# Kernel tuning notes

Measured on AMD Instinct MI355X. Metric: run time of the kernel, lower is better.

The kernel has to match this reference:

```python
import jax, jax.numpy as jnp
import numpy as np

ALPHA = 0.2  # LeakyReLU negative slope


def gat_layer(x, W, a, alpha=ALPHA):
    """Multi-head dense GAT layer.
    x: (B, N, F); W: (H, F, O); a: (H, 2*O, 1).
    Returns (B, N, H*O) — ELU(head outputs) concatenated over heads.
    """
    H, F, O = W.shape
    Wh = jnp.einsum('bnf,hfo->bhno', x, W)          # (B,H,N,O)
    a_src = a[:, :O, 0]                              # (H,O)
    a_dst = a[:, O:, 0]                              # (H,O)
    s_src = jnp.einsum('bhno,ho->bhn', Wh, a_src)    # (B,H,N)
    s_dst = jnp.einsum('bhno,ho->bhn', Wh, a_dst)    # (B,H,N)
    e = s_src[..., :, None] + s_dst[..., None, :]    # (B,H,N,N)
    e = jax.nn.leaky_relu(e, negative_slope=alpha)
    att = jax.nn.softmax(e, axis=-1)                 # softmax over neighbors j
    out = jnp.einsum('bhnm,bhmo->bhno', att, Wh)     # (B,H,N,O)
    out = jax.nn.elu(out)
    B, _, N, _ = out.shape
    return jnp.transpose(out, (0, 2, 1, 3)).reshape(B, N, H * O)


def setup_inputs() -> dict:
    key = jax.random.key(0)
    ks = jax.random.split(key, 5)
    B, N = 32, 1024
    x = jax.random.normal(ks[0], (B, N, 4), dtype=jnp.float32)
    # layer1: nfeat=4, nhid=2, nheads=3
    W1 = jax.random.normal(ks[1], (3, 4, 2), dtype=jnp.float32) * 0.5
    a1 = jax.random.normal(ks[2], (3, 4, 1), dtype=jnp.float32) * 0.5
    # layer2: nfeat=6, nhid=4, nheads=1
    W2 = jax.random.normal(ks[3], (1, 6, 4), dtype=jnp.float32) * 0.5
    a2 = jax.random.normal(ks[4], (1, 8, 1), dtype=jnp.float32) * 0.5
    return {"x": x, "W1": W1, "a1": a1, "W2": W2, "a2": a2}


def reference(x, W1, a1, W2, a2):
    h = gat_layer(x, W1, a1)   # (B, N, 6)
    y = gat_layer(h, W2, a2)   # (B, N, 4)
    return y
```

## Files before the change

### kernel.cpp

```cpp
#include <hip/hip_runtime.h>


#define GAT_ALPHA 0.2f
#define LOG2E 1.44269504088896f

__device__ __forceinline__ float ex2(float v) { return __builtin_amdgcn_exp2f(v); }

template <int F, int O, int H, int NT>
__global__ __launch_bounds__(NT) void gat_bucket_kernel(
    const float* __restrict__ x,
    const float* __restrict__ Wt,
    const float* __restrict__ at,
    float* __restrict__ out)
{
    constexpr int N = 1024, EPT = N / NT;
    constexpr int NB = 512;
    constexpr int A1 = O + 1;
    constexpr int NW = NT / 64;
    constexpr int NJOBS = 2 * A1 + 1;
    constexpr int BPL = NB / 64;

    const int bid = blockIdx.x;
    const int h   = bid % H;
    const int b   = bid / H;
    const int tid = threadIdx.x;
    const int wv  = tid >> 6, ln = tid & 63;

    float Wl[F][O], asrc[O], adst[O];
#pragma unroll
    for (int f = 0; f < F; ++f)
#pragma unroll
        for (int o = 0; o < O; ++o) Wl[f][o] = Wt[(h * F + f) * O + o];
#pragma unroll
    for (int o = 0; o < O; ++o) {
        asrc[o] = at[h * 2 * O + o];
        adst[o] = at[h * 2 * O + O + o];
    }

    __shared__ float sSrc[N];
    __shared__ int   sCS[NB + 1];
    __shared__ float sKey[N];
    __shared__ float sWhS[O][N];
    __shared__ float sPre[A1][NB + 1];
    __shared__ float sSuf[A1][NB + 1];
    __shared__ float sMM[2 * NW];

    for (int i = tid; i < NB + 1; i += NT) sCS[i] = 0;
    for (int i = tid; i < A1 * (NB + 1); i += NT) {
        (&sPre[0][0])[i] = 0.0f;
        (&sSuf[0][0])[i] = 0.0f;
    }

    float key[EPT], wh[EPT][O];
    float kmin = 3.4e38f, kmax = -3.4e38f;
    const float* xb = x + (size_t)b * N * F;
#pragma unroll
    for (int k = 0; k < EPT; ++k) {
        const int m = k * NT + tid;
        float xv[F];
        if constexpr (F == 4) {
            const float4 v = ((const float4*)xb)[m];
            xv[0] = v.x; xv[1] = v.y; xv[2] = v.z; xv[3] = v.w;
        } else {
            const float2* x2 = (const float2*)xb;
            const float2 va = x2[3 * m], vb = x2[3 * m + 1], vc = x2[3 * m + 2];
            xv[0] = va.x; xv[1] = va.y; xv[2] = vb.x;
            xv[3] = vb.y; xv[4] = vc.x; xv[5] = vc.y;
        }
        float d = 0.0f, sn = 0.0f;
#pragma unroll
        for (int o = 0; o < O; ++o) {
            float acc = 0.0f;
#pragma unroll
            for (int f = 0; f < F; ++f) acc += xv[f] * Wl[f][o];
            wh[k][o] = acc;
            d += acc * adst[o];
            sn += acc * asrc[o];
        }
        key[k] = d;
        sSrc[m] = sn;
        kmin = fminf(kmin, d);
        kmax = fmaxf(kmax, d);
    }
#pragma unroll
    for (int s = 1; s < 64; s <<= 1) {
        kmin = fminf(kmin, __shfl_xor(kmin, s, 64));
        kmax = fmaxf(kmax, __shfl_xor(kmax, s, 64));
    }
    if (ln == 0) { sMM[wv] = kmin; sMM[NW + wv] = kmax; }
    __syncthreads();

    kmin = sMM[0]; kmax = sMM[NW];
#pragma unroll
    for (int w = 1; w < NW; ++w) {
        kmin = fminf(kmin, sMM[w]);
        kmax = fmaxf(kmax, sMM[NW + w]);
    }
    const float invw = (float)NB / fmaxf(kmax - kmin, 1e-30f);

    int bk[EPT], rk[EPT];
#pragma unroll
    for (int k = 0; k < EPT; ++k) {
        int q = (int)((key[k] - kmin) * invw);
        q = q < 0 ? 0 : (q > NB - 1 ? NB - 1 : q);
        bk[k] = q;
        rk[k] = atomicAdd(&sCS[q], 1);
        const float e1 = ex2(LOG2E * key[k]);
        const float e2 = ex2(GAT_ALPHA * LOG2E * key[k]);
        atomicAdd(&sSuf[0][q], e1);
        atomicAdd(&sPre[0][q], e2);
#pragma unroll
        for (int o = 0; o < O; ++o) {
            atomicAdd(&sSuf[1 + o][q], e1 * wh[k][o]);
            atomicAdd(&sPre[1 + o][q], e2 * wh[k][o]);
        }
    }
    __syncthreads();

    if (wv < NJOBS) {
        if (wv == 0) {
            int c[BPL];
#pragma unroll
            for (int i = 0; i < BPL; ++i) c[i] = sCS[ln * BPL + i];
            int s = 0;
#pragma unroll
            for (int i = 0; i < BPL; ++i) s += c[i];
            int run = s;
#pragma unroll
            for (int d = 1; d < 64; d <<= 1) {
                const int u = __shfl_up(run, d, 64);
                if (ln >= d) run += u;
            }
            int acc = run - s;
#pragma unroll
            for (int i = 0; i < BPL; ++i) {
                const int t = acc; acc += c[i];
                sCS[ln * BPL + i] = t;
            }
            if (ln == 0) sCS[NB] = N;
        } else if (wv <= A1) {
            float* arr = &sPre[wv - 1][0];
            float v[BPL];
#pragma unroll
            for (int i = 0; i < BPL; ++i) v[i] = arr[ln * BPL + i];
            float s = 0.0f;
#pragma unroll
            for (int i = 0; i < BPL; ++i) s += v[i];
            float run = s;
#pragma unroll
            for (int d = 1; d < 64; d <<= 1) {
                const float u = __shfl_up(run, d, 64);
                if (ln >= d) run += u;
            }
            float acc = run - s;
#pragma unroll
            for (int i = 0; i < BPL; ++i) {
                const float t = acc; acc += v[i];
                arr[ln * BPL + i] = t;
            }
        } else {
            float* arr = &sSuf[wv - A1 - 1][0];
            float v[BPL];
#pragma unroll
            for (int i = 0; i < BPL; ++i) v[i] = arr[ln * BPL + i];
            float s = 0.0f;
#pragma unroll
            for (int i = 0; i < BPL; ++i) s += v[i];
            float run = s;
#pragma unroll
            for (int d = 1; d < 64; d <<= 1) {
                const float u = __shfl_down(run, d, 64);
                if (ln < 64 - d) run += u;
            }
            float acc = run - s;
#pragma unroll
            for (int i = BPL - 1; i >= 0; --i) {
                acc += v[i];
                arr[ln * BPL + i] = acc;
            }
        }
    }
    __syncthreads();

#pragma unroll
    for (int k = 0; k < EPT; ++k) {
        const int pos = sCS[bk[k]] + rk[k];
        sKey[pos] = key[k];
#pragma unroll
        for (int o = 0; o < O; ++o) sWhS[o][pos] = wh[k][o];
    }
    __syncthreads();

    for (int rr = tid; rr < N; rr += NT) {
        const float sn = sSrc[rr];
        const float rho = ex2(0.8f * LOG2E * sn);
        int bq = (int)((-sn - kmin) * invw);
        bq = bq < 0 ? 0 : (bq > NB - 1 ? NB - 1 : bq);
        const int i0 = sCS[bq], i1 = sCS[bq + 1];
        float den = rho * sSuf[0][bq + 1] + sPre[0][bq];
        float num[O];
#pragma unroll
        for (int o = 0; o < O; ++o)
            num[o] = rho * sSuf[1 + o][bq + 1] + sPre[1 + o][bq];
        for (int i = i0; i < i1; ++i) {
            const float kk = sKey[i];
            const float w = fmaxf(rho * ex2(LOG2E * kk), ex2(GAT_ALPHA * LOG2E * kk));
            den += w;
#pragma unroll
            for (int o = 0; o < O; ++o) num[o] += w * sWhS[o][i];
        }
#pragma unroll
        for (int o = 0; o < O; ++o) {
            float v = num[o] / den;
            v = (v > 0.0f) ? v : (__expf(v) - 1.0f);
            out[((size_t)b * N + rr) * (H * O) + h * O + o] = v;
        }
    }
}

extern "C" void kernel_launch(void* const* d_in, const int* in_sizes, int n_in,
                              void* d_out, int out_size, void* d_ws, size_t ws_size,
                              hipStream_t stream) {
    const float* x  = (const float*)d_in[0];
    const float* W1 = (const float*)d_in[1];
    const float* a1 = (const float*)d_in[2];
    const float* W2 = (const float*)d_in[3];
    const float* a2 = (const float*)d_in[4];

    float* h1 = (float*)d_ws;
    float* y  = (float*)d_out;

    constexpr int B = 32;
    gat_bucket_kernel<4, 2, 3, 1024><<<B * 3, 1024, 0, stream>>>(x, W1, a1, h1);
    gat_bucket_kernel<6, 4, 1, 1024><<<B * 1, 1024, 0, stream>>>(h1, W2, a2, y);
}
```

Baseline: 91.51 us.

## Fuse both GAT layers into one per-batch kernel with aliased shared memory

Merges the two layer launches into a single kernel with one block per batch element. That block computes all three layer-1 heads, keeps the layer-1 output in registers, and then runs layer 2, so the global-memory round trip of the hidden activations and one launch go away. In layer 1 the bucket stage stores only sorted node indices and recomputes Wh and the key from x inside the within-bucket loop, which saves shared memory so three heads fit and layer 2 can reuse the same region. The cost is parallelism: only 32 blocks run instead of 96 for layer 1, which leaves most CUs idle, and the recompute adds gathered global reads in the inner loop.

Result: slower. 114.2 us (+24.8%).

```diff
diff --git a/kernel.cpp b/kernel.cpp
--- a/kernel.cpp
+++ b/kernel.cpp
@@ -6,215 +6,323 @@
 
 __device__ __forceinline__ float ex2(float v) { return __builtin_amdgcn_exp2f(v); }
 
-template <int F, int O, int H, int NT>
-__global__ __launch_bounds__(NT) void gat_bucket_kernel(
+constexpr int N = 1024, NT = 1024, NW = NT / 64, NB = 512, BPL = NB / 64;
+constexpr int WCS = NB + 1;
+
+constexpr int OFF_PRE1 = WCS;
+constexpr int OFF_SUF1 = OFF_PRE1 + 3 * WCS;
+constexpr int OFF_IDX1 = OFF_SUF1 + 3 * WCS;
+constexpr int L1_HEAD  = OFF_IDX1 + N;
+constexpr int L1_ZERO  = OFF_IDX1;
+constexpr int SMEM_WORDS = 3 * L1_HEAD;
+
+constexpr int OFF2_KEY = WCS;
+constexpr int OFF2_WHS = OFF2_KEY + N;
+constexpr int OFF2_PRE = OFF2_WHS + 4 * N;
+constexpr int OFF2_SUF = OFF2_PRE + 5 * WCS;
+constexpr int L2_TOTAL = OFF2_SUF + 5 * WCS;
+static_assert(L2_TOTAL <= SMEM_WORDS, "L2 must alias inside L1 region");
+
+__device__ __forceinline__ void wave_scan_int(int* a, int ln) {
+    int c[BPL];
+#pragma unroll
+    for (int i = 0; i < BPL; ++i) c[i] = a[ln * BPL + i];
+    int s = 0;
+#pragma unroll
+    for (int i = 0; i < BPL; ++i) s += c[i];
+    int run = s;
+#pragma unroll
+    for (int d = 1; d < 64; d <<= 1) {
+        const int u = __shfl_up(run, d, 64);
+        if (ln >= d) run += u;
+    }
+    int acc = run - s;
+#pragma unroll
+    for (int i = 0; i < BPL; ++i) { const int t = acc; acc += c[i]; a[ln * BPL + i] = t; }
+    if (ln == 63) a[NB] = run;
+}
+__device__ __forceinline__ void wave_scan_pre(float* a, int ln) {
+    float c[BPL];
+#pragma unroll
+    for (int i = 0; i < BPL; ++i) c[i] = a[ln * BPL + i];
+    float s = 0.0f;
+#pragma unroll
+    for (int i = 0; i < BPL; ++i) s += c[i];
+    float run = s;
+#pragma unroll
+    for (int d = 1; d < 64; d <<= 1) {
+        const float u = __shfl_up(run, d, 64);
+        if (ln >= d) run += u;
+    }
+    float acc = run - s;
+#pragma unroll
+    for (int i = 0; i < BPL; ++i) { const float t = acc; acc += c[i]; a[ln * BPL + i] = t; }
+}
+__device__ __forceinline__ void wave_scan_suf(float* a, int ln) {
+    float c[BPL];
+#pragma unroll
+    for (int i = 0; i < BPL; ++i) c[i] = a[ln * BPL + i];
+    float s = 0.0f;
+#pragma unroll
+    for (int i = 0; i < BPL; ++i) s += c[i];
+    float run = s;
+#pragma unroll
+    for (int d = 1; d < 64; d <<= 1) {
+        const float u = __shfl_down(run, d, 64);
+        if (ln < 64 - d) run += u;
+    }
+    float acc = run - s;
+#pragma unroll
+    for (int i = BPL - 1; i >= 0; --i) { acc += c[i]; a[ln * BPL + i] = acc; }
+}
+
+__global__ __launch_bounds__(NT) void gat_fused(
     const float* __restrict__ x,
-    const float* __restrict__ Wt,
-    const float* __restrict__ at,
+    const float* __restrict__ W1,
+    const float* __restrict__ a1,
+    const float* __restrict__ W2,
+    const float* __restrict__ a2,
     float* __restrict__ out)
 {
-    constexpr int N = 1024, EPT = N / NT;
-    constexpr int NB = 512;
-    constexpr int A1 = O + 1;
-    constexpr int NW = NT / 64;
-    constexpr int NJOBS = 2 * A1 + 1;
-    constexpr int BPL = NB / 64;
-
-    const int bid = blockIdx.x;
-    const int h   = bid % H;
-    const int b   = bid / H;
-    const int tid = threadIdx.x;
-    const int wv  = tid >> 6, ln = tid & 63;
-
-    float Wl[F][O], asrc[O], adst[O];
-#pragma unroll
-    for (int f = 0; f < F; ++f)
-#pragma unroll
-        for (int o = 0; o < O; ++o) Wl[f][o] = Wt[(h * F + f) * O + o];
-#pragma unroll
-    for (int o = 0; o < O; ++o) {
-        asrc[o] = at[h * 2 * O + o];
-        adst[o] = at[h * 2 * O + O + o];
-    }
-
-    __shared__ float sSrc[N];
-    __shared__ int   sCS[NB + 1];
-    __shared__ float sKey[N];
-    __shared__ float sWhS[O][N];
-    __shared__ float sPre[A1][NB + 1];
-    __shared__ float sSuf[A1][NB + 1];
-    __shared__ float sMM[2 * NW];
-
-    for (int i = tid; i < NB + 1; i += NT) sCS[i] = 0;
-    for (int i = tid; i < A1 * (NB + 1); i += NT) {
-        (&sPre[0][0])[i] = 0.0f;
-        (&sSuf[0][0])[i] = 0.0f;
-    }
-
-    float key[EPT], wh[EPT][O];
-    float kmin = 3.4e38f, kmax = -3.4e38f;
-    const float* xb = x + (size_t)b * N * F;
-#pragma unroll
-    for (int k = 0; k < EPT; ++k) {
-        const int m = k * NT + tid;
-        float xv[F];
-        if constexpr (F == 4) {
-            const float4 v = ((const float4*)xb)[m];
-            xv[0] = v.x; xv[1] = v.y; xv[2] = v.z; xv[3] = v.w;
-        } else {
-            const float2* x2 = (const float2*)xb;
-            const float2 va = x2[3 * m], vb = x2[3 * m + 1], vc = x2[3 * m + 2];
-            xv[0] = va.x; xv[1] = va.y; xv[2] = vb.x;
-            xv[3] = vb.y; xv[4] = vc.x; xv[5] = vc.y;
-        }
-        float d = 0.0f, sn = 0.0f;
-#pragma unroll
-        for (int o = 0; o < O; ++o) {
-            float acc = 0.0f;
-#pragma unroll
-            for (int f = 0; f < F; ++f) acc += xv[f] * Wl[f][o];
-            wh[k][o] = acc;
-            d += acc * adst[o];
-            sn += acc * asrc[o];
-        }
-        key[k] = d;
-        sSrc[m] = sn;
-        kmin = fminf(kmin, d);
-        kmax = fmaxf(kmax, d);
-    }
-#pragma unroll
-    for (int s = 1; s < 64; s <<= 1) {
-        kmin = fminf(kmin, __shfl_xor(kmin, s, 64));
-        kmax = fmaxf(kmax, __shfl_xor(kmax, s, 64));
-    }
-    if (ln == 0) { sMM[wv] = kmin; sMM[NW + wv] = kmax; }
-    __syncthreads();
-
-    kmin = sMM[0]; kmax = sMM[NW];
-#pragma unroll
-    for (int w = 1; w < NW; ++w) {
-        kmin = fminf(kmin, sMM[w]);
-        kmax = fmaxf(kmax, sMM[NW + w]);
-    }
-    const float invw = (float)NB / fmaxf(kmax - kmin, 1e-30f);
-
-    int bk[EPT], rk[EPT];
-#pragma unroll
-    for (int k = 0; k < EPT; ++k) {
-        int q = (int)((key[k] - kmin) * invw);
+    __shared__ __align__(16) float smem[SMEM_WORDS];
+    __shared__ float sMM[4][2 * NW];
+
+    const int b   = blockIdx.x;
+    const int tid = threadIdx.x, wv = tid >> 6, ln = tid & 63;
+    const int m   = tid;
+
+    float Wl1[3][4][2], as1[3][2], ad1[3][2];
+#pragma unroll
+    for (int hh = 0; hh < 3; ++hh) {
+#pragma unroll
+        for (int f = 0; f < 4; ++f)
+#pragma unroll
+            for (int o = 0; o < 2; ++o) Wl1[hh][f][o] = W1[(hh * 4 + f) * 2 + o];
+#pragma unroll
+        for (int o = 0; o < 2; ++o) {
+            as1[hh][o] = a1[hh * 4 + o];
+            ad1[hh][o] = a1[hh * 4 + 2 + o];
+        }
+    }
+
+    const float4* xb4 = (const float4*)(x + (size_t)b * N * 4);
+
+#pragma unroll
+    for (int hh = 0; hh < 3; ++hh) {
+        float* bp = smem + hh * L1_HEAD;
+        for (int i = tid; i < L1_ZERO; i += NT) bp[i] = 0.0f;
+    }
+
+    const float4 xr = xb4[m];
+    float key1[3], sn1[3], wh1[3][2];
+#pragma unroll
+    for (int hh = 0; hh < 3; ++hh) {
+        const float w0 = xr.x * Wl1[hh][0][0] + xr.y * Wl1[hh][1][0] +
+                         xr.z * Wl1[hh][2][0] + xr.w * Wl1[hh][3][0];
+        const float w1 = xr.x * Wl1[hh][0][1] + xr.y * Wl1[hh][1][1] +
+                         xr.z * Wl1[hh][2][1] + xr.w * Wl1[hh][3][1];
+        wh1[hh][0] = w0; wh1[hh][1] = w1;
+        key1[hh] = w0 * ad1[hh][0] + w1 * ad1[hh][1];
+        sn1[hh]  = w0 * as1[hh][0] + w1 * as1[hh][1];
+        float mn = key1[hh], mx = key1[hh];
+#pragma unroll
+        for (int d = 1; d < 64; d <<= 1) {
+            mn = fminf(mn, __shfl_xor(mn, d, 64));
+            mx = fmaxf(mx, __shfl_xor(mx, d, 64));
+        }
+        if (ln == 0) { sMM[hh][wv] = mn; sMM[hh][NW + wv] = mx; }
+    }
+    __syncthreads();
+
+    float kmin1[3], invw1[3];
+#pragma unroll
+    for (int hh = 0; hh < 3; ++hh) {
+        float mn = sMM[hh][0], mx = sMM[hh][NW];
+#pragma unroll
+        for (int w = 1; w < NW; ++w) {
+            mn = fminf(mn, sMM[hh][w]);
+            mx = fmaxf(mx, sMM[hh][NW + w]);
+        }
+        kmin1[hh] = mn;
+        invw1[hh] = (float)NB / fmaxf(mx - mn, 1e-30f);
+    }
+
+    int bk1[3], rk1[3];
+#pragma unroll
+    for (int hh = 0; hh < 3; ++hh) {
+        float* bp = smem + hh * L1_HEAD;
+        int q = (int)((key1[hh] - kmin1[hh]) * invw1[hh]);
         q = q < 0 ? 0 : (q > NB - 1 ? NB - 1 : q);
-        bk[k] = q;
-        rk[k] = atomicAdd(&sCS[q], 1);
-        const float e1 = ex2(LOG2E * key[k]);
-        const float e2 = ex2(GAT_ALPHA * LOG2E * key[k]);
-        atomicAdd(&sSuf[0][q], e1);
-        atomicAdd(&sPre[0][q], e2);
-#pragma unroll
-        for (int o = 0; o < O; ++o) {
-            atomicAdd(&sSuf[1 + o][q], e1 * wh[k][o]);
-            atomicAdd(&sPre[1 + o][q], e2 * wh[k][o]);
-        }
-    }
-    __syncthreads();
-
-    if (wv < NJOBS) {
-        if (wv == 0) {
-            int c[BPL];
-#pragma unroll
-            for (int i = 0; i < BPL; ++i) c[i] = sCS[ln * BPL + i];
-            int s = 0;
-#pragma unroll
-            for (int i = 0; i < BPL; ++i) s += c[i];
-            int run = s;
-#pragma unroll
-            for (int d = 1; d < 64; d <<= 1) {
-                const int u = __shfl_up(run, d, 64);
-                if (ln >= d) run += u;
-            }
-            int acc = run - s;
-#pragma unroll
-            for (int i = 0; i < BPL; ++i) {
-                const int t = acc; acc += c[i];
-                sCS[ln * BPL + i] = t;
-            }
-            if (ln == 0) sCS[NB] = N;
-        } else if (wv <= A1) {
-            float* arr = &sPre[wv - 1][0];
-            float v[BPL];
-#pragma unroll
-            for (int i = 0; i < BPL; ++i) v[i] = arr[ln * BPL + i];
-            float s = 0.0f;
-#pragma unroll
-            for (int i = 0; i < BPL; ++i) s += v[i];
-            float run = s;
-#pragma unroll
-            for (int d = 1; d < 64; d <<= 1) {
-                const float u = __shfl_up(run, d, 64);
-                if (ln >= d) run += u;
-            }
-            float acc = run - s;
-#pragma unroll
-            for (int i = 0; i < BPL; ++i) {
-                const float t = acc; acc += v[i];
-                arr[ln * BPL + i] = t;
-            }
-        } else {
-            float* arr = &sSuf[wv - A1 - 1][0];
-            float v[BPL];
-#pragma unroll
-            for (int i = 0; i < BPL; ++i) v[i] = arr[ln * BPL + i];
-            float s = 0.0f;
-#pragma unroll
-            for (int i = 0; i < BPL; ++i) s += v[i];
-            float run = s;
-#pragma unroll
-            for (int d = 1; d < 64; d <<= 1) {
-                const float u = __shfl_down(run, d, 64);
-                if (ln < 64 - d) run += u;
-            }
-            float acc = run - s;
-#pragma unroll
-            for (int i = BPL - 1; i >= 0; --i) {
-                acc += v[i];
-                arr[ln * BPL + i] = acc;
-            }
-        }
-    }
-    __syncthreads();
-
-#pragma unroll
-    for (int k = 0; k < EPT; ++k) {
-        const int pos = sCS[bk[k]] + rk[k];
-        sKey[pos] = key[k];
-#pragma unroll
-        for (int o = 0; o < O; ++o) sWhS[o][pos] = wh[k][o];
-    }
-    __syncthreads();
-
-    for (int rr = tid; rr < N; rr += NT) {
-        const float sn = sSrc[rr];
+        bk1[hh] = q;
+        rk1[hh] = atomicAdd((int*)bp + q, 1);
+        const float e1 = ex2(LOG2E * key1[hh]);
+        const float e2 = ex2(GAT_ALPHA * LOG2E * key1[hh]);
+        atomicAdd(bp + OFF_SUF1 + q, e1);
+        atomicAdd(bp + OFF_PRE1 + q, e2);
+#pragma unroll
+        for (int o = 0; o < 2; ++o) {
+            atomicAdd(bp + OFF_SUF1 + (1 + o) * WCS + q, e1 * wh1[hh][o]);
+            atomicAdd(bp + OFF_PRE1 + (1 + o) * WCS + q, e2 * wh1[hh][o]);
+        }
+    }
+    __syncthreads();
+
+    for (int job = wv; job < 21; job += NW) {
+        const int hh = job / 7, role = job % 7;
+        float* bp = smem + hh * L1_HEAD;
+        if (role == 0)      wave_scan_int((int*)bp, ln);
+        else if (role <= 3) wave_scan_pre(bp + OFF_PRE1 + (role - 1) * WCS, ln);
+        else                wave_scan_suf(bp + OFF_SUF1 + (role - 4) * WCS, ln);
+    }
+    __syncthreads();
+
+#pragma unroll
+    for (int hh = 0; hh < 3; ++hh) {
+        float* bp = smem + hh * L1_HEAD;
+        const int pos = ((int*)bp)[bk1[hh]] + rk1[hh];
+        ((int*)bp)[OFF_IDX1 + pos] = m;
+    }
+    __syncthreads();
+
+    float hv[6];
+#pragma unroll
+    for (int hh = 0; hh < 3; ++hh) {
+        float* bp = smem + hh * L1_HEAD;
+        const int* cs = (const int*)bp;
+        const float sn = sn1[hh];
         const float rho = ex2(0.8f * LOG2E * sn);
-        int bq = (int)((-sn - kmin) * invw);
+        int bq = (int)((-sn - kmin1[hh]) * invw1[hh]);
         bq = bq < 0 ? 0 : (bq > NB - 1 ? NB - 1 : bq);
-        const int i0 = sCS[bq], i1 = sCS[bq + 1];
-        float den = rho * sSuf[0][bq + 1] + sPre[0][bq];
-        float num[O];
-#pragma unroll
-        for (int o = 0; o < O; ++o)
-            num[o] = rho * sSuf[1 + o][bq + 1] + sPre[1 + o][bq];
+        const int i0 = cs[bq], i1 = cs[bq + 1];
+        float den = rho * bp[OFF_SUF1 + bq + 1] + bp[OFF_PRE1 + bq];
+        float n0  = rho * bp[OFF_SUF1 + WCS + bq + 1] + bp[OFF_PRE1 + WCS + bq];
+        float n1  = rho * bp[OFF_SUF1 + 2 * WCS + bq + 1] + bp[OFF_PRE1 + 2 * WCS + bq];
         for (int i = i0; i < i1; ++i) {
-            const float kk = sKey[i];
+            const int mi = ((const int*)bp)[OFF_IDX1 + i];
+            const float4 xi = xb4[mi];
+            const float w0 = xi.x * Wl1[hh][0][0] + xi.y * Wl1[hh][1][0] +
+                             xi.z * Wl1[hh][2][0] + xi.w * Wl1[hh][3][0];
+            const float w1 = xi.x * Wl1[hh][0][1] + xi.y * Wl1[hh][1][1] +
+                             xi.z * Wl1[hh][2][1] + xi.w * Wl1[hh][3][1];
+            const float kk = w0 * ad1[hh][0] + w1 * ad1[hh][1];
             const float w = fmaxf(rho * ex2(LOG2E * kk), ex2(GAT_ALPHA * LOG2E * kk));
             den += w;
-#pragma unroll
-            for (int o = 0; o < O; ++o) num[o] += w * sWhS[o][i];
-        }
-#pragma unroll
-        for (int o = 0; o < O; ++o) {
+            n0 += w * w0;
+            n1 += w * w1;
+        }
+        float v0 = n0 / den, v1 = n1 / den;
+        hv[hh * 2]     = (v0 > 0.0f) ? v0 : (__expf(v0) - 1.0f);
+        hv[hh * 2 + 1] = (v1 > 0.0f) ? v1 : (__expf(v1) - 1.0f);
+    }
+    __syncthreads();
+
+    float Wl2[6][4], as2[4], ad2[4];
+#pragma unroll
+    for (int f = 0; f < 6; ++f)
+#pragma unroll
+        for (int o = 0; o < 4; ++o) Wl2[f][o] = W2[f * 4 + o];
+#pragma unroll
+    for (int o = 0; o < 4; ++o) { as2[o] = a2[o]; ad2[o] = a2[4 + o]; }
+
+    for (int i = tid; i < WCS; i += NT) ((int*)smem)[i] = 0;
+    for (int i = tid; i < 10 * WCS; i += NT) smem[OFF2_PRE + i] = 0.0f;
+
+    float key2, sn2, wh2[4];
+    {
+        float kd = 0.0f, sn = 0.0f;
+#pragma unroll
+        for (int o = 0; o < 4; ++o) {
+            float acc = 0.0f;
+#pragma unroll
+            for (int f = 0; f < 6; ++f) acc += hv[f] * Wl2[f][o];
+            wh2[o] = acc;
+            kd += acc * ad2[o];
+            sn += acc * as2[o];
+        }
+        key2 = kd; sn2 = sn;
+        float mn = kd, mx = kd;
+#pragma unroll
+        for (int d = 1; d < 64; d <<= 1) {
+            mn = fminf(mn, __shfl_xor(mn, d, 64));
+            mx = fmaxf(mx, __shfl_xor(mx, d, 64));
+        }
+        if (ln == 0) { sMM[3][wv] = mn; sMM[3][NW + wv] = mx; }
+    }
+    __syncthreads();
+
+    float kmin2, invw2;
+    {
+        float mn = sMM[3][0], mx = sMM[3][NW];
+#pragma unroll
+        for (int w = 1; w < NW; ++w) {
+            mn = fminf(mn, sMM[3][w]);
+            mx = fmaxf(mx, sMM[3][NW + w]);
+        }
+        kmin2 = mn;
+        invw2 = (float)NB / fmaxf(mx - mn, 1e-30f);
+    }
+
+    int bk2, rk2;
+    {
+        int q = (int)((key2 - kmin2) * invw2);
+        q = q < 0 ? 0 : (q > NB - 1 ? NB - 1 : q);
+        bk2 = q;
+        rk2 = atomicAdd((int*)smem + q, 1);
+        const float e1 = ex2(LOG2E * key2);
+        const float e2 = ex2(GAT_ALPHA * LOG2E * key2);
+        atomicAdd(smem + OFF2_SUF + q, e1);
+        atomicAdd(smem + OFF2_PRE + q, e2);
+#pragma unroll
+        for (int o = 0; o < 4; ++o) {
+            atomicAdd(smem + OFF2_SUF + (1 + o) * WCS + q, e1 * wh2[o]);
+            atomicAdd(smem + OFF2_PRE + (1 + o) * WCS + q, e2 * wh2[o]);
+        }
+    }
+    __syncthreads();
+
+    if (wv < 11) {
+        if (wv == 0)      wave_scan_int((int*)smem, ln);
+        else if (wv <= 5) wave_scan_pre(smem + OFF2_PRE + (wv - 1) * WCS, ln);
+        else              wave_scan_suf(smem + OFF2_SUF + (wv - 6) * WCS, ln);
+    }
+    __syncthreads();
+
+    {
+        const int pos = ((int*)smem)[bk2] + rk2;
+        smem[OFF2_KEY + pos] = key2;
+#pragma unroll
+        for (int o = 0; o < 4; ++o) smem[OFF2_WHS + o * N + pos] = wh2[o];
+    }
+    __syncthreads();
+
+    {
+        const int* cs = (const int*)smem;
+        const float rho = ex2(0.8f * LOG2E * sn2);
+        int bq = (int)((-sn2 - kmin2) * invw2);
+        bq = bq < 0 ? 0 : (bq > NB - 1 ? NB - 1 : bq);
+        const int i0 = cs[bq], i1 = cs[bq + 1];
+        float den = rho * smem[OFF2_SUF + bq + 1] + smem[OFF2_PRE + bq];
+        float num[4];
+#pragma unroll
+        for (int o = 0; o < 4; ++o)
+            num[o] = rho * smem[OFF2_SUF + (1 + o) * WCS + bq + 1] +
+                     smem[OFF2_PRE + (1 + o) * WCS + bq];
+        for (int i = i0; i < i1; ++i) {
+            const float kk = smem[OFF2_KEY + i];
+            const float w = fmaxf(rho * ex2(LOG2E * kk), ex2(GAT_ALPHA * LOG2E * kk));
+            den += w;
+#pragma unroll
+            for (int o = 0; o < 4; ++o) num[o] += w * smem[OFF2_WHS + o * N + i];
+        }
+        float vv[4];
+#pragma unroll
+        for (int o = 0; o < 4; ++o) {
             float v = num[o] / den;
-            v = (v > 0.0f) ? v : (__expf(v) - 1.0f);
-            out[((size_t)b * N + rr) * (H * O) + h * O + o] = v;
-        }
+            vv[o] = (v > 0.0f) ? v : (__expf(v) - 1.0f);
+        }
+        float4 yv;
+        yv.x = vv[0]; yv.y = vv[1]; yv.z = vv[2]; yv.w = vv[3];
+        ((float4*)out)[(size_t)b * N + m] = yv;
     }
 }
 
@@ -226,11 +334,8 @@
     const float* a1 = (const float*)d_in[2];
     const float* W2 = (const float*)d_in[3];
     const float* a2 = (const float*)d_in[4];
-
-    float* h1 = (float*)d_ws;
-    float* y  = (float*)d_out;
-
-    constexpr int B = 32;
-    gat_bucket_kernel<4, 2, 3, 1024><<<B * 3, 1024, 0, stream>>>(x, W1, a1, h1);
-    gat_bucket_kernel<6, 4, 1, 1024><<<B * 1, 1024, 0, stream>>>(h1, W2, a2, y);
-}
+    float* y = (float*)d_out;
+
+    (void)d_ws; (void)ws_size;
+    gat_fused<<<32, NT, 0, stream>>>(x, W1, a1, W2, a2, y);
+}
```
